# Kernel optimization log

Measured on AMD Instinct MI355X. Metric: run time of the kernel, lower is better.

## Reference

```python
import jax, jax.numpy as jnp
import numpy as np
from jax import lax

B, T = 8192, 128
HID = 64


def setup_inputs() -> dict:
    key = jax.random.key(0)
    ks = jax.random.split(key, 16)
    actor_ids = jax.random.randint(ks[0], (B, T), 0, 7, dtype=jnp.int32)
    action_ids = jax.random.randint(ks[1], (B, T), 0, 4, dtype=jnp.int32)
    street_ids = jax.random.randint(ks[2], (B, T), 0, 5, dtype=jnp.int32)
    bet_fraction = jax.random.uniform(ks[3], (B, T, 1), dtype=jnp.float32)
    # prefix-valid mask from random lengths (some zero-length rows)
    lengths = jax.random.randint(ks[4], (B,), 0, T + 1)
    valid_mask = jnp.arange(T)[None, :] < lengths[:, None]  # [B,T] bool
    s = 0.1
    params = {
        "E_actor": jax.random.normal(ks[5], (7, 8), jnp.float32) * s,
        "E_action": jax.random.normal(ks[6], (4, 8), jnp.float32) * s,
        "E_street": jax.random.normal(ks[7], (5, 4), jnp.float32) * s,
        "W_proj": jax.random.normal(ks[8], (32, 21), jnp.float32) * s,
        "b_proj": jax.random.normal(ks[9], (32,), jnp.float32) * s,
        "W_ih": jax.random.normal(ks[10], (3 * HID, 32), jnp.float32) * s,
        "W_hh": jax.random.normal(ks[11], (3 * HID, HID), jnp.float32) * s,
        "b_ih": jax.random.normal(ks[12], (3 * HID,), jnp.float32) * s,
        "b_hh": jax.random.normal(ks[13], (3 * HID,), jnp.float32) * s,
    }
    return dict(actor_ids=actor_ids, action_ids=action_ids, street_ids=street_ids,
                bet_fraction=bet_fraction, valid_mask=valid_mask, **params)


def reference(actor_ids, action_ids, street_ids, bet_fraction, valid_mask,
              E_actor, E_action, E_street, W_proj, b_proj,
              W_ih, W_hh, b_ih, b_hh):
    # embed + concat -> [B,T,21]
    feats = jnp.concatenate([E_actor[actor_ids], E_action[action_ids],
                             E_street[street_ids], bet_fraction], axis=-1)
    x = feats @ W_proj.T + b_proj                      # [B,T,32]
    # precompute input-side GRU gates for all timesteps: [B,T,3H]
    xg = x @ W_ih.T + b_ih
    xg_t = jnp.swapaxes(xg, 0, 1)                      # [T,B,3H]
    m_t = jnp.swapaxes(valid_mask, 0, 1)               # [T,B]

    def step(h, inp):
        xg_i, m = inp
        hg = h @ W_hh.T + b_hh                         # [B,3H]
        xr, xz, xn = jnp.split(xg_i, 3, axis=-1)
        hr, hz, hn = jnp.split(hg, 3, axis=-1)
        r = jax.nn.sigmoid(xr + hr)
        z = jax.nn.sigmoid(xz + hz)
        n = jnp.tanh(xn + r * hn)
        h_new = (1.0 - z) * n + z * h
        # only advance hidden state while t < length (prefix-valid mask);
        # final carry equals the GRU hidden at the last valid step, and rows
        # with length 0 stay at the zero init (matches torch masking).
        h = jnp.where(m[:, None], h_new, h)
        return h, None

    h0 = jnp.zeros((x.shape[0], HID), dtype=x.dtype)
    h_final, _ = lax.scan(step, h0, (xg_t, m_t))
    return h_final
```

## Files before the change

kernel.cpp:

```cpp
#include <hip/hip_runtime.h>

#define HID 64
#define TT  128
#define NROWS 8192
#define NGRP (NROWS / 16)
#define LOG2E 1.44269504088896f

typedef _Float16 half8 __attribute__((ext_vector_type(8)));
typedef float    f32x4 __attribute__((ext_vector_type(4)));


__global__ void k_len(const int* __restrict__ mask, int* __restrict__ lens) {
    const int row = blockIdx.x * 4 + (threadIdx.x >> 6);
    const int l   = threadIdx.x & 63;
    const int* mrow = mask + row * TT;
    int c = (mrow[l] != 0) + (mrow[l + 64] != 0);
    #pragma unroll
    for (int k = 32; k >= 1; k >>= 1) c += __shfl_xor(c, k);
    if (l == 0) lens[row] = c;
}

__global__ __launch_bounds__(1024) void k_sort(const int* __restrict__ lens,
                                               int* __restrict__ perm) {
    __shared__ int hist[TT + 1];
    __shared__ int offs[TT + 1];
    const int tid = threadIdx.x;
    if (tid <= TT) hist[tid] = 0;
    __syncthreads();
    int myL[8];
    #pragma unroll
    for (int i = 0; i < 8; i++) {
        myL[i] = lens[tid + 1024 * i];
        atomicAdd(&hist[myL[i]], 1);
    }
    __syncthreads();
    if (tid <= TT) {
        int s = 0;
        for (int j = 0; j < tid; j++) s += hist[j];
        offs[tid] = s;
    }
    __syncthreads();
    #pragma unroll
    for (int i = 0; i < 8; i++) {
        const int pos = atomicAdd(&offs[myL[i]], 1);
        const int d   = NROWS - 1 - pos;
        const int gd  = d >> 4, r = d & 15;
        const int b   = (gd < 256) ? gd : 767 - gd;
        perm[b * 16 + r] = tid + 1024 * i;
    }
}

__global__ __launch_bounds__(256, 2) void gru_fused(
    const int* __restrict__ actor_ids, const int* __restrict__ action_ids,
    const int* __restrict__ street_ids, const float* __restrict__ bet,
    const float* __restrict__ E_actor, const float* __restrict__ E_action,
    const float* __restrict__ E_street, const float* __restrict__ W_proj,
    const float* __restrict__ b_proj, const float* __restrict__ W_ih,
    const float* __restrict__ b_ih, const float* __restrict__ W_hh,
    const float* __restrict__ b_hh, const int* __restrict__ perm,
    const int* __restrict__ lens, float* __restrict__ out)
{
    __shared__ __align__(16) union {
        float wfs[192][32];
        struct {
            int pb[TT][17];
            __align__(16) _Float16 hb[2][16][72];
            int Lsh[16];
            int Psh[16];
        } c;
    } A;
    __shared__ __align__(16) _Float16 embl[144];
    __shared__ float bfs[192];

    const int tid = threadIdx.x;
    const int wv  = tid >> 6;
    const int l   = tid & 63;
    const int q   = l >> 4;
    const int n   = l & 15;
    const int g   = blockIdx.x;

    for (int i = tid; i < 136; i += 256) {
        int r = i >> 3, m = i & 7;
        float v = 0.f;
        if (r < 7)       v = E_actor[r * 8 + m];
        else if (r < 11) v = E_action[(r - 7) * 8 + m];
        else if (r < 16) v = (m < 4) ? E_street[(r - 11) * 4 + m] : 0.f;
        embl[i] = (_Float16)v;
    }

    if (tid < 192) {
        const int j = tid;
        float wf[21];
        #pragma unroll
        for (int m = 0; m < 21; m++) wf[m] = 0.f;
        float bf = b_ih[j];
        for (int k = 0; k < 32; k++) {
            const float w = W_ih[j * 32 + k];
            bf += w * b_proj[k];
            #pragma unroll
            for (int m = 0; m < 21; m++) wf[m] += w * W_proj[k * 21 + m];
        }
        const float s = (j < 128) ? LOG2E : 2.f * LOG2E;
        #pragma unroll
        for (int m = 0; m < 21; m++) A.wfs[j][m] = wf[m] * s;
        #pragma unroll
        for (int m = 21; m < 32; m++) A.wfs[j][m] = 0.f;
        bfs[j] = bf;
    }
    __syncthreads();

    half8 Af[3], Ah[3][2];
    {
        const int m16 = l & 15, kq = l >> 4;
        #pragma unroll
        for (int g3 = 0; g3 < 3; g3++) {
            const int jr = g3 * 64 + wv * 16 + m16;
            _Float16 v[8];
            #pragma unroll
            for (int m = 0; m < 8; m++) v[m] = (_Float16)A.wfs[jr][kq * 8 + m];
            Af[g3] = *(half8*)v;
            const float s = (g3 < 2) ? LOG2E : 2.f * LOG2E;
            #pragma unroll
            for (int kt = 0; kt < 2; kt++) {
                _Float16 w[8];
                #pragma unroll
                for (int m = 0; m < 8; m++)
                    w[m] = (_Float16)(W_hh[jr * HID + kt * 32 + kq * 8 + m] * s);
                Ah[g3][kt] = *(half8*)w;
            }
        }
    }
    f32x4 biasR, biasZ, biasX, biasH;
    #pragma unroll
    for (int e = 0; e < 4; e++) {
        const int idx = 16 * wv + 4 * q + e;
        biasR[e] = (bfs[idx]      + b_hh[idx])      * LOG2E;
        biasZ[e] = (bfs[64 + idx] + b_hh[64 + idx]) * LOG2E;
        biasX[e] = bfs[128 + idx]  * (2.f * LOG2E);
        biasH[e] = b_hh[128 + idx] * (2.f * LOG2E);
    }
    __syncthreads();

    for (int i = tid; i < 2 * 16 * 72 / 2; i += 256) ((int*)A.c.hb)[i] = 0;
    {
        const int r = tid >> 4, tl = tid & 15;
        const int prow = perm[g * 16 + r];
        const int base = prow * TT;
        #pragma unroll
        for (int i = 0; i < 8; i++) {
            const int t = tl + 16 * i;
            const int a = actor_ids[base + t], c = action_ids[base + t];
            const int s = street_ids[base + t];
            const _Float16 f16 = (_Float16)bet[base + t];
            const unsigned fb = (unsigned)*(const unsigned short*)&f16;
            A.c.pb[t][r] = (int)(a | (c << 3) | (s << 5) | (fb << 16));
        }
        if (tl == 0) { A.c.Lsh[r] = lens[prow]; A.c.Psh[r] = prow; }
    }
    __syncthreads();

    const int Ln = A.c.Lsh[n];
    int Lmax = Ln;
    #pragma unroll
    for (int k = 1; k < 16; k <<= 1) {
        const int o = __shfl_xor(Lmax, k);
        Lmax = (o > Lmax) ? o : Lmax;
    }

    const bool isq2 = (q == 2);
    const int sh = (q == 1) ? 3 : (q == 2) ? 5 : 0;
    const int mk = (q == 1) ? 3 : (q == 3) ? 0 : 7;
    const int of = (q == 1) ? 7 : (q == 2) ? 11 : (q == 3) ? 16 : 0;

    float h[4] = {0.f, 0.f, 0.f, 0.f};
    const f32x4 zero4 = {0.f, 0.f, 0.f, 0.f};

    f32x4 xR, xZ, xX;
    half8 Bfn;
    {
        const int p0 = A.c.pb[0][n];
        const int e0 = ((p0 >> sh) & mk) + of;
        half8 Bf0 = *(const half8*)&embl[e0 * 8];
        uint4* b0 = (uint4*)&Bf0;
        b0->z = isq2 ? ((unsigned)p0 >> 16) : b0->z;
        xR = __builtin_amdgcn_mfma_f32_16x16x32_f16(Af[0], Bf0, biasR, 0, 0, 0);
        xZ = __builtin_amdgcn_mfma_f32_16x16x32_f16(Af[1], Bf0, biasZ, 0, 0, 0);
        xX = __builtin_amdgcn_mfma_f32_16x16x32_f16(Af[2], Bf0, biasX, 0, 0, 0);

        const int p1 = A.c.pb[1][n];
        const int e1 = ((p1 >> sh) & mk) + of;
        half8 Bf1 = *(const half8*)&embl[e1 * 8];
        uint4* b1 = (uint4*)&Bf1;
        b1->z = isq2 ? ((unsigned)p1 >> 16) : b1->z;
        Bfn = Bf1;
    }

    for (int t = 0; t < Lmax; t++) {
        const int buf = t & 1;
        const half8 Bh0 = *(const half8*)&A.c.hb[buf][n][q * 8];
        const half8 Bh1 = *(const half8*)&A.c.hb[buf][n][32 + q * 8];
        const int t2 = (t + 2 < TT) ? t + 2 : TT - 1;
        const int p2 = A.c.pb[t2][n];

        f32x4 aRa = __builtin_amdgcn_mfma_f32_16x16x32_f16(Ah[0][0], Bh0, xR, 0, 0, 0);
        f32x4 aRb = __builtin_amdgcn_mfma_f32_16x16x32_f16(Ah[0][1], Bh1, zero4, 0, 0, 0);
        f32x4 aZ = __builtin_amdgcn_mfma_f32_16x16x32_f16(Ah[1][0], Bh0, xZ, 0, 0, 0);
        aZ = __builtin_amdgcn_mfma_f32_16x16x32_f16(Ah[1][1], Bh1, aZ, 0, 0, 0);
        f32x4 aH = __builtin_amdgcn_mfma_f32_16x16x32_f16(Ah[2][0], Bh0, biasH, 0, 0, 0);
        aH = __builtin_amdgcn_mfma_f32_16x16x32_f16(Ah[2][1], Bh1, aH, 0, 0, 0);
        const f32x4 aR = aRa + aRb;
        const f32x4 aXc = xX;

        const f32x4 xRn = __builtin_amdgcn_mfma_f32_16x16x32_f16(Af[0], Bfn, biasR, 0, 0, 0);
        const f32x4 xZn = __builtin_amdgcn_mfma_f32_16x16x32_f16(Af[1], Bfn, biasZ, 0, 0, 0);
        const f32x4 xXn = __builtin_amdgcn_mfma_f32_16x16x32_f16(Af[2], Bfn, biasX, 0, 0, 0);

        half8 Bf2;
        {
            const int e2 = ((p2 >> sh) & mk) + of;
            Bf2 = *(const half8*)&embl[e2 * 8];
            uint4* b2 = (uint4*)&Bf2;
            b2->z = isq2 ? ((unsigned)p2 >> 16) : b2->z;
        }

        const bool live = (t < Ln);
        _Float16 hp[4];
        #pragma unroll
        for (int e = 0; e < 4; e++) {
            const float r = __builtin_amdgcn_rcpf(1.f + __builtin_amdgcn_exp2f(-aR[e]));
            const float z = __builtin_amdgcn_rcpf(1.f + __builtin_amdgcn_exp2f(-aZ[e]));
            const float y2 = aXc[e] + r * aH[e];
            const float nn = 1.f - 2.f * __builtin_amdgcn_rcpf(1.f + __builtin_amdgcn_exp2f(y2));
            const float hv = nn + z * (h[e] - nn);
            h[e] = live ? hv : h[e];
            hp[e] = (_Float16)h[e];
        }
        *(uint2*)&A.c.hb[buf ^ 1][n][16 * wv + 4 * q] = *(uint2*)hp;
        __syncthreads();

        xR = xRn; xZ = xZn; xX = xXn; Bfn = Bf2;
    }

    const int prow = A.c.Psh[n];
    float4 o = make_float4(h[0], h[1], h[2], h[3]);
    *(float4*)&out[prow * HID + 16 * wv + 4 * q] = o;
}

extern "C" void kernel_launch(void* const* d_in, const int* in_sizes, int n_in,
                              void* d_out, int out_size, void* d_ws, size_t ws_size,
                              hipStream_t stream) {
    const int*   actor_ids  = (const int*)d_in[0];
    const int*   action_ids = (const int*)d_in[1];
    const int*   street_ids = (const int*)d_in[2];
    const float* bet        = (const float*)d_in[3];
    const int*   vmask      = (const int*)d_in[4];
    const float* E_actor    = (const float*)d_in[5];
    const float* E_action   = (const float*)d_in[6];
    const float* E_street   = (const float*)d_in[7];
    const float* W_proj     = (const float*)d_in[8];
    const float* b_proj     = (const float*)d_in[9];
    const float* W_ih       = (const float*)d_in[10];
    const float* W_hh       = (const float*)d_in[11];
    const float* b_ih       = (const float*)d_in[12];
    const float* b_hh       = (const float*)d_in[13];
    float*       out        = (float*)d_out;

    int* ws   = (int*)d_ws;
    int* lens = ws;
    int* perm = ws + NROWS;

    k_len<<<NROWS / 4, 256, 0, stream>>>(vmask, lens);
    k_sort<<<1, 1024, 0, stream>>>(lens, perm);

    gru_fused<<<NGRP, 256, 0, stream>>>(actor_ids, action_ids, street_ids, bet,
                                        E_actor, E_action, E_street,
                                        W_proj, b_proj, W_ih, b_ih, W_hh, b_hh,
                                        perm, lens, out);
}
```

Baseline: 168.6 us.

## Split GRU gate elementwise work across paired waves with 512-thread blocks

Doubles the block to 8 waves, so each pair of waves computes the same 16-column MFMA tiles redundantly. Each wave of the pair then evaluates only two of the four accumulator elements through the sigmoid/tanh chain. The aim is to shorten the serial transcendental latency in each recurrent step. In exchange, MFMA issue per CU doubles, each step's barrier now spans 8 waves, and the 512/4 launch bound squeezes the register budget.

```diff
diff --git a/kernel.cpp b/kernel.cpp
--- a/kernel.cpp
+++ b/kernel.cpp
@@ -50,7 +50,7 @@
     }
 }
 
-__global__ __launch_bounds__(256, 2) void gru_fused(
+__global__ __launch_bounds__(512, 4) void gru_fused(
     const int* __restrict__ actor_ids, const int* __restrict__ action_ids,
     const int* __restrict__ street_ids, const float* __restrict__ bet,
     const float* __restrict__ E_actor, const float* __restrict__ E_action,
@@ -72,14 +72,16 @@
     __shared__ __align__(16) _Float16 embl[144];
     __shared__ float bfs[192];
 
-    const int tid = threadIdx.x;
-    const int wv  = tid >> 6;
-    const int l   = tid & 63;
-    const int q   = l >> 4;
-    const int n   = l & 15;
-    const int g   = blockIdx.x;
-
-    for (int i = tid; i < 136; i += 256) {
+    const int tid  = threadIdx.x;
+    const int wv   = tid >> 6;
+    const int p    = wv >> 1;
+    const int half = wv & 1;
+    const int l    = tid & 63;
+    const int q    = l >> 4;
+    const int n    = l & 15;
+    const int g    = blockIdx.x;
+
+    for (int i = tid; i < 136; i += 512) {
         int r = i >> 3, m = i & 7;
         float v = 0.f;
         if (r < 7)       v = E_actor[r * 8 + m];
@@ -114,7 +116,7 @@
         const int m16 = l & 15, kq = l >> 4;
         #pragma unroll
         for (int g3 = 0; g3 < 3; g3++) {
-            const int jr = g3 * 64 + wv * 16 + m16;
+            const int jr = g3 * 64 + p * 16 + m16;
             _Float16 v[8];
             #pragma unroll
             for (int m = 0; m < 8; m++) v[m] = (_Float16)A.wfs[jr][kq * 8 + m];
@@ -133,7 +135,7 @@
     f32x4 biasR, biasZ, biasX, biasH;
     #pragma unroll
     for (int e = 0; e < 4; e++) {
-        const int idx = 16 * wv + 4 * q + e;
+        const int idx = 16 * p + 4 * q + e;
         biasR[e] = (bfs[idx]      + b_hh[idx])      * LOG2E;
         biasZ[e] = (bfs[64 + idx] + b_hh[64 + idx]) * LOG2E;
         biasX[e] = bfs[128 + idx]  * (2.f * LOG2E);
@@ -141,14 +143,14 @@
     }
     __syncthreads();
 
-    for (int i = tid; i < 2 * 16 * 72 / 2; i += 256) ((int*)A.c.hb)[i] = 0;
+    for (int i = tid; i < 2 * 16 * 72 / 2; i += 512) ((int*)A.c.hb)[i] = 0;
     {
-        const int r = tid >> 4, tl = tid & 15;
+        const int r = tid >> 5, tl = tid & 31;
         const int prow = perm[g * 16 + r];
         const int base = prow * TT;
         #pragma unroll
-        for (int i = 0; i < 8; i++) {
-            const int t = tl + 16 * i;
+        for (int i = 0; i < 4; i++) {
+            const int t = tl + 32 * i;
             const int a = actor_ids[base + t], c = action_ids[base + t];
             const int s = street_ids[base + t];
             const _Float16 f16 = (_Float16)bet[base + t];
@@ -172,7 +174,8 @@
     const int mk = (q == 1) ? 3 : (q == 3) ? 0 : 7;
     const int of = (q == 1) ? 7 : (q == 2) ? 11 : (q == 3) ? 16 : 0;
 
-    float h[4] = {0.f, 0.f, 0.f, 0.f};
+    const int j0 = 16 * p + 4 * q + 2 * half;
+    float h0 = 0.f, h1 = 0.f;
     const f32x4 zero4 = {0.f, 0.f, 0.f, 0.f};
 
     f32x4 xR, xZ, xX;
@@ -223,27 +226,40 @@
             b2->z = isq2 ? ((unsigned)p2 >> 16) : b2->z;
         }
 
+        const float vR0 = half ? aR[2]  : aR[0],  vR1 = half ? aR[3]  : aR[1];
+        const float vZ0 = half ? aZ[2]  : aZ[0],  vZ1 = half ? aZ[3]  : aZ[1];
+        const float vH0 = half ? aH[2]  : aH[0],  vH1 = half ? aH[3]  : aH[1];
+        const float vX0 = half ? aXc[2] : aXc[0], vX1 = half ? aXc[3] : aXc[1];
+
         const bool live = (t < Ln);
-        _Float16 hp[4];
-        #pragma unroll
-        for (int e = 0; e < 4; e++) {
-            const float r = __builtin_amdgcn_rcpf(1.f + __builtin_amdgcn_exp2f(-aR[e]));
-            const float z = __builtin_amdgcn_rcpf(1.f + __builtin_amdgcn_exp2f(-aZ[e]));
-            const float y2 = aXc[e] + r * aH[e];
-            const float nn = 1.f - 2.f * __builtin_amdgcn_rcpf(1.f + __builtin_amdgcn_exp2f(y2));
-            const float hv = nn + z * (h[e] - nn);
-            h[e] = live ? hv : h[e];
-            hp[e] = (_Float16)h[e];
-        }
-        *(uint2*)&A.c.hb[buf ^ 1][n][16 * wv + 4 * q] = *(uint2*)hp;
+        {
+            const float r0 = __builtin_amdgcn_rcpf(1.f + __builtin_amdgcn_exp2f(-vR0));
+            const float z0 = __builtin_amdgcn_rcpf(1.f + __builtin_amdgcn_exp2f(-vZ0));
+            const float y0 = vX0 + r0 * vH0;
+            const float n0 = 1.f - 2.f * __builtin_amdgcn_rcpf(1.f + __builtin_amdgcn_exp2f(y0));
+            const float hv0 = n0 + z0 * (h0 - n0);
+            h0 = live ? hv0 : h0;
+
+            const float r1 = __builtin_amdgcn_rcpf(1.f + __builtin_amdgcn_exp2f(-vR1));
+            const float z1 = __builtin_amdgcn_rcpf(1.f + __builtin_amdgcn_exp2f(-vZ1));
+            const float y1 = vX1 + r1 * vH1;
+            const float n1 = 1.f - 2.f * __builtin_amdgcn_rcpf(1.f + __builtin_amdgcn_exp2f(y1));
+            const float hv1 = n1 + z1 * (h1 - n1);
+            h1 = live ? hv1 : h1;
+        }
+        {
+            const _Float16 a16 = (_Float16)h0, b16 = (_Float16)h1;
+            const unsigned pk = (unsigned)*(const unsigned short*)&a16 |
+                                ((unsigned)*(const unsigned short*)&b16 << 16);
+            *(unsigned*)&A.c.hb[buf ^ 1][n][j0] = pk;
+        }
         __syncthreads();
 
         xR = xRn; xZ = xZn; xX = xXn; Bfn = Bf2;
     }
 
     const int prow = A.c.Psh[n];
-    float4 o = make_float4(h[0], h[1], h[2], h[3]);
-    *(float4*)&out[prow * HID + 16 * wv + 4 * q] = o;
+    *(float2*)&out[prow * HID + j0] = make_float2(h0, h1);
 }
 
 extern "C" void kernel_launch(void* const* d_in, const int* in_sizes, int n_in,
@@ -272,7 +288,7 @@
     k_len<<<NROWS / 4, 256, 0, stream>>>(vmask, lens);
     k_sort<<<1, 1024, 0, stream>>>(lens, perm);
 
-    gru_fused<<<NGRP, 256, 0, stream>>>(actor_ids, action_ids, street_ids, bet,
+    gru_fused<<<NGRP, 512, 0, stream>>>(actor_ids, action_ids, street_ids, bet,
                                         E_actor, E_action, E_street,
                                         W_proj, b_proj, W_ih, b_ih, W_hh, b_hh,
                                         perm, lens, out);
```

Result: no change. 168.1 us (-0.3%).
